# Performance work log

Hardware: AMD Instinct MI355X
Metric: run time of the kernel (lower is better)

## Reference

```python
import jax, jax.numpy as jnp
import numpy as np

B = 1024
IN = 512      # in_features
O = 64        # out_features
E = 8         # ensamble
K = O * E     # total tiny MLPs, index k = i*E + j (i: output, j: ensemble)


def setup_inputs() -> dict:
    key = jax.random.key(0)
    k1, k2, k3, k4, k5 = jax.random.split(key, 5)
    s = 1.0 / np.sqrt(IN)
    X = jax.random.normal(k1, (B, IN), dtype=jnp.float32)
    # Stacked weights for all K = O*E tiny MLPs.
    # nn.Linear(in,in): y = x @ W1^T + b1, W1: [in_out, in_in]
    W1 = jax.random.uniform(k2, (K, IN, IN), jnp.float32, -s, s)
    b1 = jax.random.uniform(k3, (K, IN), jnp.float32, -s, s)
    # nn.Linear(in,1): W2 squeezed to [K, IN], b2 to [K]
    W2 = jax.random.uniform(k4, (K, IN), jnp.float32, -s, s)
    b2 = jax.random.uniform(k5, (K,), jnp.float32, -s, s)
    return {"X": X, "W1": W1, "b1": b1, "W2": W2, "b2": b2}


def reference(X, W1, b1, W2, b2):
    # h[b,k,:] = relu(X[b] @ W1[k].T + b1[k])  -- one batched GEMM
    h = jax.nn.relu(jnp.einsum('bi,kji->bkj', X, W1) + b1)  # [B,K,IN]
    out = jnp.einsum('bkj,kj->bk', h, W2) + b2              # [B,K]
    # original: concat over ensemble (dim=-1) then stack over out_features (dim=-1)
    out = out.reshape(X.shape[0], O, E).transpose(0, 2, 1)  # [B,E,O]
    return out
```

## Files before the change

### kernel.cpp

```cpp
#include <hip/hip_runtime.h>
#include <hip/hip_bf16.h>

typedef __attribute__((ext_vector_type(8))) short short8;
typedef __attribute__((ext_vector_type(4))) float f32x4;

__device__ __forceinline__ short8 pack8(const f32x4& a, const f32x4& b) {
    union { __hip_bfloat162 h[4]; short8 s; } u;
    u.h[0] = __float22bfloat162_rn(make_float2(a[0], a[1]));
    u.h[1] = __float22bfloat162_rn(make_float2(a[2], a[3]));
    u.h[2] = __float22bfloat162_rn(make_float2(b[0], b[1]));
    u.h[3] = __float22bfloat162_rn(make_float2(b[2], b[3]));
    return u.s;
}

__device__ __forceinline__ int swz4(int g) { return g ^ (((g >> 4) & 3) << 1); }

#define GLDS(GP, LP)                                                          \
    __builtin_amdgcn_global_load_lds(                                         \
        (__attribute__((address_space(1))) void*)(void*)(GP),                 \
        (__attribute__((address_space(3))) void*)(void*)(LP), 16, 0, 0)

__global__ __launch_bounds__(256)
void ens_cvt(const float* __restrict__ X, const float* __restrict__ W1,
             short* __restrict__ WS)
{
    const int t = threadIdx.x, lane = t & 63, wv = t >> 6;
    const int g = blockIdx.x * 4 + wv;
    const int row16 = lane & 15, koct = lane >> 4;
    const float* src;
    short* dst;
    if (blockIdx.x < 4096) {
        const int km = g >> 5, f = g & 31;
        src = W1 + (size_t)km * 262144 + (size_t)(f * 16 + row16) * 512 + koct * 8;
        dst = WS + (size_t)km * 262144 + (size_t)(f * 16) * 512 + lane * 8;
    } else {
        const int mf = g - 16384;
        src = X + (size_t)(mf * 16 + row16) * 512 + koct * 8;
        dst = WS + 134217728ull + (size_t)(mf * 16) * 512 + lane * 8;
    }
#pragma unroll
    for (int ks = 0; ks < 16; ++ks) {
        f32x4 a = *(const f32x4*)(src + ks * 32);
        f32x4 b = *(const f32x4*)(src + ks * 32 + 4);
        *(short8*)(dst + ks * 512) = pack8(a, b);
    }
}

#define SB __builtin_amdgcn_sched_barrier(0)

#define RDA4(DST, MI0, KKV)                                                   \
    _Pragma("unroll") for (int ii = 0; ii < 4; ++ii)                          \
        DST[ii] = *(const short8*)(rb +                                       \
            (((wm * 8 + (MI0) + ii) * 2 + (KKV)) << 10) + l16);

#define RDB4(DST, KKV)                                                        \
    _Pragma("unroll") for (int pp = 0; pp < 4; ++pp)                          \
        DST[pp] = *(const short8*)(rb + 32768 +                               \
            (((wn * 4 + pp) * 2 + (KKV)) << 10) + l16);

#define MFMA16(AV, BV, AOFF)                                                  \
    __builtin_amdgcn_s_setprio(1);                                            \
    _Pragma("unroll") for (int ii = 0; ii < 4; ++ii)                          \
        _Pragma("unroll") for (int pp = 0; pp < 4; ++pp)                      \
            acc[(AOFF) + ii][pp] = __builtin_amdgcn_mfma_f32_16x16x32_bf16(   \
                AV[ii], BV[pp], acc[(AOFF) + ii][pp], 0, 0, 0);               \
    __builtin_amdgcn_s_setprio(0);

#define GLDS4A(KOFF)                                                          \
    GLDS(gsrc + (KOFF) + 0,     wdst + 0);                                    \
    GLDS(gsrc + (KOFF) + 512,   wdst + 1024);                                 \
    GLDS(gsrc + (KOFF) + 8192,  wdst + 2048);                                 \
    GLDS(gsrc + (KOFF) + 8704,  wdst + 3072);

#define GLDS4B(KOFF)                                                          \
    GLDS(gsrc + (KOFF) + 16384, wdst + 4096);                                 \
    GLDS(gsrc + (KOFF) + 16896, wdst + 5120);                                 \
    GLDS(gsrc + (KOFF) + 24576, wdst + 6144);                                 \
    GLDS(gsrc + (KOFF) + 25088, wdst + 7168);

__global__ __launch_bounds__(512, 2)
void ens_gemm_dma(const short* __restrict__ Xb, const short* __restrict__ W1b,
                  const float* __restrict__ B1, const float* __restrict__ W2,
                  const float* __restrict__ B2, float* __restrict__ out)
{
    extern __shared__ char smem[];
    const int t    = threadIdx.x;
    const int lane = t & 63;
    const int l16  = lane << 4;
    const int wv   = t >> 6;
    const int wm   = wv >> 2;
    const int wn   = wv & 3;

    const int bb  = blockIdx.x;
    const int xcd = bb & 7;
    const int j   = bb >> 3;
    const int km  = xcd * 64 + (j >> 3);
    const int sub = j & 7;
    const int mt  = sub >> 1;
    const int nt  = sub & 1;

    const short* gsrc;
    int wvoff;
    if (wv < 4) {
        gsrc  = Xb + (size_t)(mt * 16 + wv * 4) * 8192 + lane * 8;
        wvoff = wv * 8192;
    } else {
        gsrc  = W1b + (size_t)km * 262144 +
                (size_t)(nt * 16 + (wv - 4) * 4) * 8192 + lane * 8;
        wvoff = 32768 + (wv - 4) * 8192;
    }

    f32x4 acc[8][4];
#pragma unroll
    for (int i = 0; i < 8; ++i)
#pragma unroll
        for (int p = 0; p < 4; ++p)
            acc[i][p] = (f32x4)0.0f;

    short8 avP[4], avQ[4], avR[4];
    short8 bvP[4], bvQ[4];

    {
        char* wdst = smem + wvoff;
        GLDS4A(0);
        GLDS4B(0);
        asm volatile("s_waitcnt vmcnt(0)" ::: "memory");
        SB;
        __builtin_amdgcn_s_barrier();
    }

#pragma unroll 1
    for (int kt = 0; kt < 8; ++kt) {
        const char* rb = smem + (kt & 1) * 65536;
        char* wdst     = smem + ((kt + 1) & 1) * 65536 + wvoff;
        const int koff = (kt + 1) << 10;
        const bool stage = (kt < 7);

        RDA4(avP, 0, 0);
        RDB4(bvP, 0);
        SB;
        RDA4(avQ, 4, 0);
        SB;
        if (stage) { GLDS4A(koff); }
        asm volatile("s_waitcnt lgkmcnt(4)" ::: "memory");
        SB;
        MFMA16(avP, bvP, 0);
        SB;

        RDA4(avR, 0, 1);
        RDB4(bvQ, 1);
        SB;
        if (stage) { GLDS4B(koff); }
        asm volatile("s_waitcnt lgkmcnt(8)" ::: "memory");
        SB;
        MFMA16(avQ, bvP, 4);
        SB;

        RDA4(avP, 4, 1);
        SB;
        asm volatile("s_waitcnt lgkmcnt(4)" ::: "memory");
        SB;
        MFMA16(avR, bvQ, 0);
        SB;

        asm volatile("s_waitcnt lgkmcnt(0)" ::: "memory");
        if (stage) { asm volatile("s_waitcnt vmcnt(0)" ::: "memory"); }
        SB;
        MFMA16(avP, bvQ, 4);
        SB;
        __builtin_amdgcn_s_barrier();
    }

    const int nc = lane & 15;
    const int kq = lane >> 4;
    float b1v[4], w2v[4];
#pragma unroll
    for (int pp = 0; pp < 4; ++pp) {
        int n = nt * 256 + (wn * 4 + pp) * 16 + nc;
        b1v[pp] = B1[km * 512 + n];
        w2v[pp] = W2[km * 512 + n];
    }

    float* lout = (float*)smem;
#pragma unroll
    for (int i = 0; i < 8; ++i) {
#pragma unroll
        for (int r = 0; r < 4; ++r) {
            float s = 0.f;
#pragma unroll
            for (int pp = 0; pp < 4; ++pp) {
                float h = acc[i][pp][r] + b1v[pp];
                h = h > 0.f ? h : 0.f;
                s += h * w2v[pp];
            }
#pragma unroll
            for (int d = 1; d < 16; d <<= 1)
                s += __shfl_xor(s, d, 64);
            if (nc == 0) {
                int row = wm * 128 + i * 16 + kq * 4 + r;
                lout[row * 4 + wn] = s;
            }
        }
    }
    __syncthreads();
    if (t < 256) {
        float s = lout[t * 4 + 0] + lout[t * 4 + 1] + lout[t * 4 + 2] + lout[t * 4 + 3];
        if (nt == 0) s += B2[km];
        int b = mt * 256 + t;
        atomicAdd(out + (size_t)b * 512 + (km & 7) * 64 + (km >> 3), s);
    }
}

#define FISSUE(S, BASE, KT1)                                                  \
  do {                                                                        \
    const float* q_ = (BASE) + (KT1) * 64;                                    \
    S[0] = *(const f32x4*)q_;          S[1] = *(const f32x4*)(q_ + 4);        \
    S[2] = *(const f32x4*)(q_ + 32);   S[3] = *(const f32x4*)(q_ + 36);       \
    const float* q2_ = q_ + 65536;                                            \
    S[4] = *(const f32x4*)q2_;         S[5] = *(const f32x4*)(q2_ + 4);       \
    S[6] = *(const f32x4*)(q2_ + 32);  S[7] = *(const f32x4*)(q2_ + 36);      \
  } while (0)

#define FWRITEB(S, WB, OPOFF)                                                 \
  do {                                                                        \
    char* d0_ = (WB) + (OPOFF) + wfrag;                                       \
    *(short8*)d0_ = pack8(S[0], S[1]);                                        \
    *(short8*)(d0_ + 1024) = pack8(S[2], S[3]);                               \
    char* d1_ = d0_ + 16384;                                                  \
    *(short8*)d1_ = pack8(S[4], S[5]);                                        \
    *(short8*)(d1_ + 1024) = pack8(S[6], S[7]);                               \
  } while (0)

#define FKK(RB, KKV)                                                          \
  do {                                                                        \
    _Pragma("unroll") for (int mi = 0; mi < 8; ++mi)                          \
        av[mi] = *(const short8*)((RB) +                                      \
            (((wm * 8 + mi) * 2 + (KKV)) << 10) + rdo);                       \
    _Pragma("unroll") for (int pp = 0; pp < 4; ++pp)                          \
        bv[pp] = *(const short8*)((RB) + 32768 +                              \
            (((wn * 4 + pp) * 2 + (KKV)) << 10) + rdo);                       \
    __builtin_amdgcn_s_setprio(1);                                            \
    _Pragma("unroll") for (int mi = 0; mi < 8; ++mi)                          \
        _Pragma("unroll") for (int pp = 0; pp < 4; ++pp)                      \
            acc[mi][pp] = __builtin_amdgcn_mfma_f32_16x16x32_bf16(            \
                av[mi], bv[pp], acc[mi][pp], 0, 0, 0);                        \
    __builtin_amdgcn_s_setprio(0);                                            \
  } while (0)

#define FPRO_WRITE(TT, ROFF)                                                  \
  do {                                                                        \
    short8 a_ = pack8(TT[0], TT[1]);                                          \
    short8 b_ = pack8(TT[2], TT[3]);                                          \
    char* d_ = smem + (ROFF) + wfrag;                                         \
    *(short8*)d_ = a_;                                                        \
    *(short8*)(d_ + 1024) = b_;                                               \
  } while (0)

__global__ __launch_bounds__(512, 2)
void ens_mlp_fallback(const float* __restrict__ X,
                      const float* __restrict__ W1,
                      const float* __restrict__ B1,
                      const float* __restrict__ W2,
                      const float* __restrict__ B2,
                      float* __restrict__ out)
{
    extern __shared__ char smem[];
    const int t    = threadIdx.x;
    const int lane = t & 63;
    const int wv   = t >> 6;
    const int wm   = wv >> 2;
    const int wn   = wv & 3;

    const int bb  = blockIdx.x;
    const int xcd = bb & 7;
    const int j   = bb >> 3;
    const int km  = xcd * 64 + (j >> 3);
    const int sub = j & 7;
    const int mt  = sub >> 1;
    const int nt  = sub & 1;

    const float* __restrict__ W1k = W1 + (size_t)km * (512 * 512);

    const int lr = t >> 2;
    const int c  = t & 3;
    const float* As = X   + (size_t)(mt * 256 + lr) * 512 + c * 8;
    const float* Bs = W1k + (size_t)(nt * 256 + lr) * 512 + c * 8;
    const int wfrag = ((lr >> 4) << 11) + (swz4((c << 4) | (lr & 15)) << 4);
    const int rdo   = swz4(lane) << 4;

    {
        f32x4 t0[4], t1[4], t2[4], t3[4];
        const float* q;
        q = As;          t0[0]=*(const f32x4*)q; t0[1]=*(const f32x4*)(q+4); t0[2]=*(const f32x4*)(q+32); t0[3]=*(const f32x4*)(q+36);
        q = As + 65536;  t1[0]=*(const f32x4*)q; t1[1]=*(const f32x4*)(q+4); t1[2]=*(const f32x4*)(q+32); t1[3]=*(const f32x4*)(q+36);
        q = Bs;          t2[0]=*(const f32x4*)q; t2[1]=*(const f32x4*)(q+4); t2[2]=*(const f32x4*)(q+32); t2[3]=*(const f32x4*)(q+36);
        q = Bs + 65536;  t3[0]=*(const f32x4*)q; t3[1]=*(const f32x4*)(q+4); t3[2]=*(const f32x4*)(q+32); t3[3]=*(const f32x4*)(q+36);
        asm volatile("s_waitcnt vmcnt(12)" ::: "memory"); FPRO_WRITE(t0, 0);
        asm volatile("s_waitcnt vmcnt(8)"  ::: "memory"); FPRO_WRITE(t1, 16384);
        asm volatile("s_waitcnt vmcnt(4)"  ::: "memory"); FPRO_WRITE(t2, 32768);
        asm volatile("s_waitcnt vmcnt(0)"  ::: "memory"); FPRO_WRITE(t3, 49152);
        asm volatile("s_waitcnt lgkmcnt(0)" ::: "memory");
        __builtin_amdgcn_sched_barrier(0);
        __builtin_amdgcn_s_barrier();
    }

    f32x4 acc[8][4];
#pragma unroll
    for (int i = 0; i < 8; ++i)
#pragma unroll
        for (int p = 0; p < 4; ++p)
            acc[i][p] = (f32x4)0.0f;

    short8 av[8], bv[4];
    f32x4 sS[8];

#pragma unroll 1
    for (int kt = 0; kt < 7; ++kt) {
        const char* rb = smem + (kt & 1) * 65536;
        char* wb       = smem + ((kt + 1) & 1) * 65536;

        FISSUE(sS, Bs, kt + 1);
        FKK(rb, 0);
        asm volatile("s_waitcnt vmcnt(0)" ::: "memory");
        FWRITEB(sS, wb, 32768);
        FISSUE(sS, As, kt + 1);
        FKK(rb, 1);
        asm volatile("s_waitcnt vmcnt(0)" ::: "memory");
        FWRITEB(sS, wb, 0);
        asm volatile("s_waitcnt lgkmcnt(0)" ::: "memory");
        __builtin_amdgcn_sched_barrier(0);
        __builtin_amdgcn_s_barrier();
    }
    {
        const char* rb = smem + 65536;
        FKK(rb, 0);
        FKK(rb, 1);
    }

    const int nc = lane & 15;
    const int kq = lane >> 4;
    float b1v[4], w2v[4];
#pragma unroll
    for (int pp = 0; pp < 4; ++pp) {
        int n = nt * 256 + (wn * 4 + pp) * 16 + nc;
        b1v[pp] = B1[km * 512 + n];
        w2v[pp] = W2[km * 512 + n];
    }

    float* lout = (float*)smem;
#pragma unroll
    for (int i = 0; i < 8; ++i) {
#pragma unroll
        for (int r = 0; r < 4; ++r) {
            float s = 0.f;
#pragma unroll
            for (int pp = 0; pp < 4; ++pp) {
                float h = acc[i][pp][r] + b1v[pp];
                h = h > 0.f ? h : 0.f;
                s += h * w2v[pp];
            }
#pragma unroll
            for (int d = 1; d < 16; d <<= 1)
                s += __shfl_xor(s, d, 64);
            if (nc == 0) {
                int row = wm * 128 + i * 16 + kq * 4 + r;
                lout[row * 4 + wn] = s;
            }
        }
    }
    __syncthreads();
    if (t < 256) {
        float s = lout[t * 4 + 0] + lout[t * 4 + 1] + lout[t * 4 + 2] + lout[t * 4 + 3];
        if (nt == 0) s += B2[km];
        int b = mt * 256 + t;
        atomicAdd(out + (size_t)b * 512 + (km & 7) * 64 + (km >> 3), s);
    }
}

extern "C" void kernel_launch(void* const* d_in, const int* in_sizes, int n_in,
                              void* d_out, int out_size, void* d_ws, size_t ws_size,
                              hipStream_t stream) {
    const float* X  = (const float*)d_in[0];
    const float* W1 = (const float*)d_in[1];
    const float* B1 = (const float*)d_in[2];
    const float* W2 = (const float*)d_in[3];
    const float* B2 = (const float*)d_in[4];
    float* out = (float*)d_out;

    hipMemsetAsync(out, 0, (size_t)out_size * sizeof(float), stream);

    const size_t NEED = 269484032ull;
    if (ws_size >= NEED) {
        short* WS = (short*)d_ws;
        ens_cvt<<<dim3(4112), dim3(256), 0, stream>>>(X, W1, WS);
        ens_gemm_dma<<<dim3(4096), dim3(512), 131072, stream>>>(
            WS + 134217728ull, WS, B1, W2, B2, out);
    } else {
        ens_mlp_fallback<<<dim3(4096), dim3(512), 131072, stream>>>(
            X, W1, B1, W2, B2, out);
    }
}
```

Before: 473.8 us.

## Load X operand directly to registers and halve LDS to raise occupancy

The GEMM kernel stops staging the X (A) tile through LDS. Each wave now loads its A fragments straight from global memory into registers, prefetching one k-step ahead, while only W1 (B) tiles go through LDS double buffering. That halves dynamic shared memory from 128KB to 64KB, which can allow more resident blocks per CU and reduces LDS traffic. The epilogue is also reworked to use fewer shuffles and a vectorized LDS reduction. In exchange the kernel carries more VGPR pressure and repeats global/L2 reads of X across waves, and the vmcnt accounting is intricate.

```diff
diff --git a/kernel.cpp b/kernel.cpp
--- a/kernel.cpp
+++ b/kernel.cpp
@@ -48,35 +48,22 @@
 
 #define SB __builtin_amdgcn_sched_barrier(0)
 
-#define RDA4(DST, MI0, KKV)                                                   \
-    _Pragma("unroll") for (int ii = 0; ii < 4; ++ii)                          \
-        DST[ii] = *(const short8*)(rb +                                       \
-            (((wm * 8 + (MI0) + ii) * 2 + (KKV)) << 10) + l16);
-
-#define RDB4(DST, KKV)                                                        \
+#define LOADAV(DST, AOFF)                                                     \
+    _Pragma("unroll") for (int mi = 0; mi < 8; ++mi)                          \
+        DST[mi] = *(const short8*)(pa + mi * 8192 + (AOFF));
+
+#define RDB(DST, KKV)                                                         \
     _Pragma("unroll") for (int pp = 0; pp < 4; ++pp)                          \
-        DST[pp] = *(const short8*)(rb + 32768 +                               \
+        DST[pp] = *(const short8*)(rb +                                       \
             (((wn * 4 + pp) * 2 + (KKV)) << 10) + l16);
 
-#define MFMA16(AV, BV, AOFF)                                                  \
+#define MFMA16H(AV, A0, BV)                                                   \
     __builtin_amdgcn_s_setprio(1);                                            \
     _Pragma("unroll") for (int ii = 0; ii < 4; ++ii)                          \
         _Pragma("unroll") for (int pp = 0; pp < 4; ++pp)                      \
-            acc[(AOFF) + ii][pp] = __builtin_amdgcn_mfma_f32_16x16x32_bf16(   \
-                AV[ii], BV[pp], acc[(AOFF) + ii][pp], 0, 0, 0);               \
+            acc[(A0) + ii][pp] = __builtin_amdgcn_mfma_f32_16x16x32_bf16(     \
+                AV[(A0) + ii], BV[pp], acc[(A0) + ii][pp], 0, 0, 0);          \
     __builtin_amdgcn_s_setprio(0);
-
-#define GLDS4A(KOFF)                                                          \
-    GLDS(gsrc + (KOFF) + 0,     wdst + 0);                                    \
-    GLDS(gsrc + (KOFF) + 512,   wdst + 1024);                                 \
-    GLDS(gsrc + (KOFF) + 8192,  wdst + 2048);                                 \
-    GLDS(gsrc + (KOFF) + 8704,  wdst + 3072);
-
-#define GLDS4B(KOFF)                                                          \
-    GLDS(gsrc + (KOFF) + 16384, wdst + 4096);                                 \
-    GLDS(gsrc + (KOFF) + 16896, wdst + 5120);                                 \
-    GLDS(gsrc + (KOFF) + 24576, wdst + 6144);                                 \
-    GLDS(gsrc + (KOFF) + 25088, wdst + 7168);
 
 __global__ __launch_bounds__(512, 2)
 void ens_gemm_dma(const short* __restrict__ Xb, const short* __restrict__ W1b,
@@ -99,16 +86,9 @@
     const int mt  = sub >> 1;
     const int nt  = sub & 1;
 
-    const short* gsrc;
-    int wvoff;
-    if (wv < 4) {
-        gsrc  = Xb + (size_t)(mt * 16 + wv * 4) * 8192 + lane * 8;
-        wvoff = wv * 8192;
-    } else {
-        gsrc  = W1b + (size_t)km * 262144 +
-                (size_t)(nt * 16 + (wv - 4) * 4) * 8192 + lane * 8;
-        wvoff = 32768 + (wv - 4) * 8192;
-    }
+    const short* pa = Xb + (size_t)(mt * 16 + wm * 8) * 8192 + lane * 8;
+    const short* gsrc = W1b + (size_t)km * 262144 +
+                        (size_t)(nt * 16 + wv * 2) * 8192 + lane * 8;
 
     f32x4 acc[8][4];
 #pragma unroll
@@ -117,58 +97,65 @@
         for (int p = 0; p < 4; ++p)
             acc[i][p] = (f32x4)0.0f;
 
-    short8 avP[4], avQ[4], avR[4];
+    short8 avP[8], avQ[8];
     short8 bvP[4], bvQ[4];
 
     {
-        char* wdst = smem + wvoff;
-        GLDS4A(0);
-        GLDS4B(0);
-        asm volatile("s_waitcnt vmcnt(0)" ::: "memory");
+        char* wdst = smem + wv * 4096;
+        GLDS(gsrc, wdst);            GLDS(gsrc + 512, wdst + 1024);
+        GLDS(gsrc + 8192, wdst + 2048); GLDS(gsrc + 8704, wdst + 3072);
+        SB;
+        LOADAV(avP, 0);
+        SB;
+        asm volatile("s_waitcnt vmcnt(8)" ::: "memory");
         SB;
         __builtin_amdgcn_s_barrier();
     }
 
 #pragma unroll 1
     for (int kt = 0; kt < 8; ++kt) {
-        const char* rb = smem + (kt & 1) * 65536;
-        char* wdst     = smem + ((kt + 1) & 1) * 65536 + wvoff;
+        const char* rb = smem + (kt & 1) * 32768;
+        char* wdst     = smem + ((kt + 1) & 1) * 32768 + wv * 4096;
         const int koff = (kt + 1) << 10;
         const bool stage = (kt < 7);
 
-        RDA4(avP, 0, 0);
-        RDB4(bvP, 0);
-        SB;
-        RDA4(avQ, 4, 0);
-        SB;
-        if (stage) { GLDS4A(koff); }
-        asm volatile("s_waitcnt lgkmcnt(4)" ::: "memory");
-        SB;
-        MFMA16(avP, bvP, 0);
-        SB;
-
-        RDA4(avR, 0, 1);
-        RDB4(bvQ, 1);
-        SB;
-        if (stage) { GLDS4B(koff); }
-        asm volatile("s_waitcnt lgkmcnt(8)" ::: "memory");
-        SB;
-        MFMA16(avQ, bvP, 4);
-        SB;
-
-        RDA4(avP, 4, 1);
-        SB;
-        asm volatile("s_waitcnt lgkmcnt(4)" ::: "memory");
-        SB;
-        MFMA16(avR, bvQ, 0);
-        SB;
-
+        LOADAV(avQ, (kt << 10) + 512);
+        SB;
+        RDB(bvP, 0);
+        SB;
+        if (stage) { GLDS(gsrc + koff, wdst); GLDS(gsrc + koff + 512, wdst + 1024); }
+        SB;
+        if (stage) { asm volatile("s_waitcnt vmcnt(10)" ::: "memory"); }
+        else       { asm volatile("s_waitcnt vmcnt(8)"  ::: "memory"); }
         asm volatile("s_waitcnt lgkmcnt(0)" ::: "memory");
-        if (stage) { asm volatile("s_waitcnt vmcnt(0)" ::: "memory"); }
-        SB;
-        MFMA16(avP, bvQ, 4);
-        SB;
-        __builtin_amdgcn_s_barrier();
+        SB;
+        MFMA16H(avP, 0, bvP);
+        SB;
+
+        RDB(bvQ, 1);
+        SB;
+        if (stage) { GLDS(gsrc + koff + 8192, wdst + 2048);
+                     GLDS(gsrc + koff + 8704, wdst + 3072); }
+        SB;
+        MFMA16H(avP, 4, bvP);
+        SB;
+
+        if (stage) { LOADAV(avP, (kt + 1) << 10); }
+        SB;
+        if (stage) { asm volatile("s_waitcnt vmcnt(12)" ::: "memory"); }
+        else       { asm volatile("s_waitcnt vmcnt(0)"  ::: "memory"); }
+        asm volatile("s_waitcnt lgkmcnt(0)" ::: "memory");
+        SB;
+        MFMA16H(avQ, 0, bvQ);
+        SB;
+
+        MFMA16H(avQ, 4, bvQ);
+        SB;
+        if (stage) {
+            asm volatile("s_waitcnt vmcnt(8)" ::: "memory");
+            SB;
+            __builtin_amdgcn_s_barrier();
+        }
     }
 
     const int nc = lane & 15;
@@ -193,21 +180,26 @@
                 h = h > 0.f ? h : 0.f;
                 s += h * w2v[pp];
             }
-#pragma unroll
-            for (int d = 1; d < 16; d <<= 1)
-                s += __shfl_xor(s, d, 64);
-            if (nc == 0) {
+            s += __shfl_xor(s, 1, 64);
+            s += __shfl_xor(s, 2, 64);
+            if ((nc & 3) == 0) {
                 int row = wm * 128 + i * 16 + kq * 4 + r;
-                lout[row * 4 + wn] = s;
+                lout[row * 20 + wn * 4 + (nc >> 2)] = s;
             }
         }
     }
     __syncthreads();
-    if (t < 256) {
-        float s = lout[t * 4 + 0] + lout[t * 4 + 1] + lout[t * 4 + 2] + lout[t * 4 + 3];
-        if (nt == 0) s += B2[km];
-        int b = mt * 256 + t;
-        atomicAdd(out + (size_t)b * 512 + (km & 7) * 64 + (km >> 3), s);
+    {
+        int row = t >> 1, half = t & 1;
+        const f32x4* p = (const f32x4*)(lout + row * 20 + half * 8);
+        f32x4 a = p[0], b = p[1];
+        float s = a[0] + a[1] + a[2] + a[3] + b[0] + b[1] + b[2] + b[3];
+        s += __shfl_xor(s, 1, 64);
+        if (half == 0) {
+            if (nt == 0) s += B2[km];
+            int bo = mt * 256 + row;
+            atomicAdd(out + (size_t)bo * 512 + (km & 7) * 64 + (km >> 3), s);
+        }
     }
 }
 
@@ -393,7 +385,7 @@
     if (ws_size >= NEED) {
         short* WS = (short*)d_ws;
         ens_cvt<<<dim3(4112), dim3(256), 0, stream>>>(X, W1, WS);
-        ens_gemm_dma<<<dim3(4096), dim3(512), 131072, stream>>>(
+        ens_gemm_dma<<<dim3(4096), dim3(512), 65536, stream>>>(
             WS + 134217728ull, WS, B1, W2, B2, out);
     } else {
         ens_mlp_fallback<<<dim3(4096), dim3(512), 131072, stream>>>(
```

Result: slower. 495.8 us (+4.6%).
